# Optimization experiments

Measured on AMD Instinct MI355X. Metric: run time of the kernel, lower is better.

Reference implementation:

```python
import jax, jax.numpy as jnp
import numpy as np

N = 8192          # num_nodes (feature dim == node count, x is square)
H = N // 2        # hidden channels of conv1
NUM_GRAPHS = 8    # graphs in the batch for global_mean_pool
EDGE_P = 0.004    # adjacency density -> avg degree ~33


def setup_inputs() -> dict:
    key = jax.random.key(0)
    kx, kb, k1, k2 = jax.random.split(key, 4)
    # sparse binary adjacency-as-features: nonzero(x) defines the edge list
    x = (jax.random.uniform(kx, (N, N)) < EDGE_P).astype(jnp.float32)
    batch = jnp.sort(jax.random.randint(kb, (N,), 0, NUM_GRAPHS))
    # GCNConv weights (lin has no bias in PyG; separate additive bias)
    W1 = jax.random.normal(k1, (N, H), jnp.float32) / np.sqrt(N)
    b1 = jnp.zeros((H,), jnp.float32)
    W2 = jax.random.normal(k2, (H, N), jnp.float32) / np.sqrt(H)
    b2 = jnp.zeros((N,), jnp.float32)
    return {"x": x, "W1": W1, "b1": b1, "W2": W2, "b2": b2, "batch": batch}


def _gcn_norm_adj(x):
    """Symmetric-normalized adjacency implied by edge_index = nonzero(x).

    PyG GCNConv: edges (r -> c) for every nonzero x[r, c], unit edge weight,
    remaining self loops added, deg = in-degree of target, message to node c is
    deg^-1/2[r] * deg^-1/2[c] * xw[r]. Since x is square/dense we express the
    aggregation as a dense normalized-adjacency matmul (identical math).
    """
    A = (x != 0).astype(x.dtype)                # [N, N], A[r, c] = edge r->c
    idx = jnp.arange(A.shape[0])
    A = A.at[idx, idx].set(1.0)                 # add (remaining) self loops
    deg = A.sum(axis=0)                         # in-degree of each target node
    dinv = jax.lax.rsqrt(deg)                   # deg >= 1 (self loops)
    return dinv[:, None] * A * dinv[None, :]    # B[r, c] = dinv[r]*A[r,c]*dinv[c]


def reference(x, W1, b1, W2, b2, batch):
    B = _gcn_norm_adj(x)
    # conv1: aggregate_c sum_r B[r, c] * (x @ W1)[r]  == B.T @ (x @ W1)
    h = jax.nn.relu(B.T @ (x @ W1) + b1)        # [N, H]
    h = B.T @ (h @ W2) + b2                     # [N, N]
    # global_mean_pool over graph assignment `batch`
    sums = jax.ops.segment_sum(h, batch, num_segments=NUM_GRAPHS)
    cnt = jax.ops.segment_sum(jnp.ones((h.shape[0],), h.dtype), batch,
                              num_segments=NUM_GRAPHS)
    return sums / jnp.maximum(cnt, 1.0)[:, None]  # [NUM_GRAPHS, N]
```

## Files before the change

### kernel.cpp

```cpp
#include <hip/hip_runtime.h>
#include <hip/hip_bf16.h>

#define NN 8192
#define HH 4096
#define GG 8
#define STR 128
#define NCH 32
#define PRG 64
#define FJG 32

typedef unsigned uint4n __attribute__((ext_vector_type(4)));

__device__ inline unsigned bf16rne(float f) {
    unsigned u = __float_as_uint(f);
    unsigned r = 0x7fffu + ((u >> 16) & 1u);
    return (u + r) >> 16;
}
__device__ inline unsigned pack2(float lo, float hi) {
    return bf16rne(lo) | (bf16rne(hi) << 16);
}
__device__ inline void nt_store16(void* p, unsigned a, unsigned b, unsigned c, unsigned d) {
    uint4n v; v.x = a; v.y = b; v.z = c; v.w = d;
    __builtin_nontemporal_store(v, reinterpret_cast<uint4n*>(p));
}
__device__ inline void acc2p(float2& acc, unsigned u) {
    float2 t;
    t.x = __uint_as_float(u << 16);
    t.y = __uint_as_float(u & 0xffff0000u);
    asm("v_pk_add_f32 %0, %1, %0" : "+v"(acc) : "v"(t));
}
__device__ inline void unpack8(uint4 v, float* __restrict__ h) {
    const unsigned* pu = reinterpret_cast<const unsigned*>(&v);
    #pragma unroll
    for (int q = 0; q < 4; ++q) {
        const unsigned u = pu[q];
        h[2 * q]     = __uint_as_float(u << 16);
        h[2 * q + 1] = __uint_as_float(u & 0xffff0000u);
    }
}

__global__ __launch_bounds__(256) void k_cvt(const float* __restrict__ src,
                                             uint4* __restrict__ dst) {
    const size_t i = (size_t)blockIdx.x * 256 + threadIdx.x;
    const float4 a = reinterpret_cast<const float4*>(src)[2 * i];
    const float4 b = reinterpret_cast<const float4*>(src)[2 * i + 1];
    nt_store16(&dst[i], pack2(a.x, a.y), pack2(a.z, a.w),
                        pack2(b.x, b.y), pack2(b.z, b.w));
}

__global__ __launch_bounds__(256) void k_build(const float* __restrict__ x,
                                               unsigned* __restrict__ colfill,
                                               unsigned* __restrict__ degX,
                                               unsigned* __restrict__ degA,
                                               unsigned* __restrict__ csrX,
                                               unsigned* __restrict__ csrA,
                                               unsigned* __restrict__ cscA) {
    const int r = blockIdx.x;
    __shared__ unsigned px, pa;
    if (threadIdx.x == 0) { px = 0u; pa = 0u; }
    __syncthreads();
    const float4* xr = reinterpret_cast<const float4*>(x + (size_t)r * NN);
    #pragma unroll
    for (int i = 0; i < NN / (4 * 256); ++i) {
        const int c4 = i * 256 + threadIdx.x;
        float4 v = xr[c4];
        const float* vp = reinterpret_cast<const float*>(&v);
        #pragma unroll
        for (int k = 0; k < 4; ++k) {
            const int c = c4 * 4 + k;
            const bool nzx = (vp[k] != 0.0f);
            const bool nzA = nzx || (c == r);
            if (nzx) {
                unsigned p = atomicAdd(&px, 1u);
                if (p < STR) csrX[(size_t)r * STR + p] = (unsigned)c << 13;
            }
            if (nzA) {
                unsigned p = atomicAdd(&pa, 1u);
                if (p < STR) csrA[(size_t)r * STR + p] = (unsigned)c;
                unsigned q = atomicAdd(&colfill[c], 1u);
                if (q < STR) cscA[(size_t)c * STR + q] = (unsigned)r << 13;
            }
        }
    }
    __syncthreads();
    if (threadIdx.x == 0) { degX[r] = px; degA[r] = pa; }
}

__global__ __launch_bounds__(256) void k_s(const unsigned* __restrict__ degA,
                                           const unsigned* __restrict__ csrA,
                                           const unsigned* __restrict__ colfill,
                                           const int* __restrict__ batch,
                                           float* __restrict__ s,
                                           unsigned* __restrict__ cnt) {
    const int r = blockIdx.x * 256 + threadIdx.x;
    atomicAdd(&cnt[batch[r]], 1u);
    unsigned deg = degA[r];
    if (deg > STR) deg = STR;
    float bins[GG];
    #pragma unroll
    for (int g = 0; g < GG; ++g) bins[g] = 0.0f;
    for (unsigned e = 0; e < deg; ++e) {
        const unsigned c = csrA[(size_t)r * STR + e];
        const float d = rsqrtf((float)colfill[c]);
        const int gb = batch[c];
        #pragma unroll
        for (int g = 0; g < GG; ++g) bins[g] += (gb == g) ? d : 0.0f;
    }
    const float dr = rsqrtf((float)colfill[r]);
    #pragma unroll
    for (int g = 0; g < GG; ++g) s[(size_t)g * NN + r] = dr * bins[g];
}

__global__ __launch_bounds__(256) void k_spmm1(const char* __restrict__ W1b,
                                               const unsigned* __restrict__ degX,
                                               const unsigned* __restrict__ csrX,
                                               const unsigned* __restrict__ colfill,
                                               unsigned* __restrict__ Mh) {
    const unsigned L = blockIdx.x;
    const int xcd = L & 7;
    const int pix = L >> 3;
    int node = (pix << 2) | (threadIdx.x >> 6);
    node = __builtin_amdgcn_readfirstlane(node);
    const int lane = threadIdx.x & 63;

    unsigned deg = degX[node];
    if (deg > STR) deg = STR;
    const unsigned* __restrict__ el = csrX + (size_t)node * STR;
    const float dr = rsqrtf((float)colfill[node]);

    #pragma unroll
    for (int p = 0; p < 4; ++p) {
        const int ch = xcd + (p << 3);
        const unsigned loff = (unsigned)(ch * 64 + lane) * 4u;
        float2 acc = make_float2(0.f, 0.f);
        unsigned e = 0;
        for (; e + 8 <= deg; e += 8) {
            unsigned o0 = el[e + 0], o1 = el[e + 1], o2 = el[e + 2], o3 = el[e + 3];
            unsigned o4 = el[e + 4], o5 = el[e + 5], o6 = el[e + 6], o7 = el[e + 7];
            const unsigned v0 = *reinterpret_cast<const unsigned*>(W1b + (o0 + loff));
            const unsigned v1 = *reinterpret_cast<const unsigned*>(W1b + (o1 + loff));
            const unsigned v2 = *reinterpret_cast<const unsigned*>(W1b + (o2 + loff));
            const unsigned v3 = *reinterpret_cast<const unsigned*>(W1b + (o3 + loff));
            const unsigned v4 = *reinterpret_cast<const unsigned*>(W1b + (o4 + loff));
            const unsigned v5 = *reinterpret_cast<const unsigned*>(W1b + (o5 + loff));
            const unsigned v6 = *reinterpret_cast<const unsigned*>(W1b + (o6 + loff));
            const unsigned v7 = *reinterpret_cast<const unsigned*>(W1b + (o7 + loff));
            acc2p(acc, v0); acc2p(acc, v1); acc2p(acc, v2); acc2p(acc, v3);
            acc2p(acc, v4); acc2p(acc, v5); acc2p(acc, v6); acc2p(acc, v7);
        }
        for (; e < deg; ++e) {
            unsigned o = el[e];
            acc2p(acc, *reinterpret_cast<const unsigned*>(W1b + (o + loff)));
        }
        __builtin_nontemporal_store(pack2(dr * acc.x, dr * acc.y),
                                    &Mh[(size_t)node * (HH / 2) + ch * 64 + lane]);
    }
}

__global__ __launch_bounds__(256) void k_conv1(const char* __restrict__ Mb,
                                               const float* __restrict__ b1,
                                               const unsigned* __restrict__ colfill,
                                               const unsigned* __restrict__ cscA,
                                               unsigned* __restrict__ hB) {
    const unsigned L = blockIdx.x;
    const int xcd = L & 7;
    const int pix = L >> 3;
    int node = (pix << 2) | (threadIdx.x >> 6);
    node = __builtin_amdgcn_readfirstlane(node);
    const int lane = threadIdx.x & 63;

    unsigned deg = colfill[node];
    const float dc = rsqrtf((float)deg);
    if (deg > STR) deg = STR;
    const unsigned* __restrict__ el = cscA + (size_t)node * STR;

    #pragma unroll
    for (int p = 0; p < 4; ++p) {
        const int ch = xcd + (p << 3);
        const unsigned loff = (unsigned)(ch * 64 + lane) * 4u;
        float2 acc = make_float2(0.f, 0.f);
        unsigned e = 0;
        for (; e + 8 <= deg; e += 8) {
            unsigned o0 = el[e + 0], o1 = el[e + 1], o2 = el[e + 2], o3 = el[e + 3];
            unsigned o4 = el[e + 4], o5 = el[e + 5], o6 = el[e + 6], o7 = el[e + 7];
            const unsigned v0 = *reinterpret_cast<const unsigned*>(Mb + (o0 + loff));
            const unsigned v1 = *reinterpret_cast<const unsigned*>(Mb + (o1 + loff));
            const unsigned v2 = *reinterpret_cast<const unsigned*>(Mb + (o2 + loff));
            const unsigned v3 = *reinterpret_cast<const unsigned*>(Mb + (o3 + loff));
            const unsigned v4 = *reinterpret_cast<const unsigned*>(Mb + (o4 + loff));
            const unsigned v5 = *reinterpret_cast<const unsigned*>(Mb + (o5 + loff));
            const unsigned v6 = *reinterpret_cast<const unsigned*>(Mb + (o6 + loff));
            const unsigned v7 = *reinterpret_cast<const unsigned*>(Mb + (o7 + loff));
            acc2p(acc, v0); acc2p(acc, v1); acc2p(acc, v2); acc2p(acc, v3);
            acc2p(acc, v4); acc2p(acc, v5); acc2p(acc, v6); acc2p(acc, v7);
        }
        for (; e < deg; ++e) {
            unsigned o = el[e];
            acc2p(acc, *reinterpret_cast<const unsigned*>(Mb + (o + loff)));
        }
        const float2 bv = reinterpret_cast<const float2*>(b1)[ch * 64 + lane];
        const float h0 = fmaxf(fmaf(dc, acc.x, bv.x), 0.0f);
        const float h1 = fmaxf(fmaf(dc, acc.y, bv.y), 0.0f);
        __builtin_nontemporal_store(pack2(h0, h1),
                                    &hB[(size_t)node * (HH / 2) + ch * 64 + lane]);
    }
}

__global__ __launch_bounds__(256) void k_poolA(const uint4* __restrict__ hB,
                                               const float* __restrict__ s,
                                               float* __restrict__ part) {
    const int j = blockIdx.x * 256 + threadIdx.x;
    const int c0 = blockIdx.y * (NN / PRG);
    __shared__ float s_t[GG * (NN / PRG)];
    for (int i = threadIdx.x; i < GG * (NN / PRG); i += 256) {
        const int g = i / (NN / PRG);
        const int cc = i % (NN / PRG);
        s_t[i] = s[(size_t)g * NN + c0 + cc];
    }
    __syncthreads();
    float tacc[GG][8];
    #pragma unroll
    for (int g = 0; g < GG; ++g)
        #pragma unroll
        for (int q = 0; q < 8; ++q) tacc[g][q] = 0.0f;
    for (int cc = 0; cc < NN / PRG; ++cc) {
        const uint4 v = hB[(size_t)(c0 + cc) * (HH / 8) + j];
        float hv[8];
        unpack8(v, hv);
        #pragma unroll
        for (int g = 0; g < GG; ++g) {
            const float sv = s_t[g * (NN / PRG) + cc];
            #pragma unroll
            for (int q = 0; q < 8; ++q) tacc[g][q] = fmaf(sv, hv[q], tacc[g][q]);
        }
    }
    float4* p4 = reinterpret_cast<float4*>(part);
    #pragma unroll
    for (int g = 0; g < GG; ++g) {
        const size_t base = ((size_t)(blockIdx.y * GG + g) * HH) / 4 + j * 2;
        p4[base]     = make_float4(tacc[g][0], tacc[g][1], tacc[g][2], tacc[g][3]);
        p4[base + 1] = make_float4(tacc[g][4], tacc[g][5], tacc[g][6], tacc[g][7]);
    }
}

__global__ __launch_bounds__(256) void k_poolB(const float* __restrict__ part,
                                               float* __restrict__ t) {
    const int idx = blockIdx.x * 256 + threadIdx.x;
    const int g = idx / (HH / 4);
    const int j4 = idx % (HH / 4);
    const float4* p4 = reinterpret_cast<const float4*>(part);
    float4 acc = make_float4(0.f, 0.f, 0.f, 0.f);
    for (int rg = 0; rg < PRG; ++rg) {
        const float4 v = p4[((size_t)(rg * GG + g) * HH) / 4 + j4];
        acc.x += v.x; acc.y += v.y; acc.z += v.z; acc.w += v.w;
    }
    reinterpret_cast<float4*>(t)[idx] = acc;
}

__global__ __launch_bounds__(256) void k_final(const float* __restrict__ W2,
                                               const float* __restrict__ t,
                                               const unsigned* __restrict__ cnt,
                                               float* __restrict__ part2) {
    __shared__ float tld[GG * 128];
    const int tj = threadIdx.x;
    const int j0 = blockIdx.y * 128;
    const int nbase = blockIdx.x * 1024;
    for (int i = threadIdx.x; i < GG * 128; i += 256) {
        const int g = i >> 7;
        const int jj = i & 127;
        unsigned c = cnt[g];
        if (c < 1u) c = 1u;
        tld[i] = t[(size_t)g * HH + j0 + jj] * (1.0f / (float)c);
    }
    __syncthreads();
    float4 acc[GG];
    #pragma unroll
    for (int g = 0; g < GG; ++g) acc[g] = make_float4(0.f, 0.f, 0.f, 0.f);
    for (int jj = 0; jj < 128; ++jj) {
        const int jv = j0 + jj;
        float4 w = reinterpret_cast<const float4*>(W2 + (size_t)jv * NN + nbase)[tj];
        #pragma unroll
        for (int g = 0; g < GG; ++g) {
            const float tv = tld[g * 128 + jj];
            acc[g].x = fmaf(tv, w.x, acc[g].x);
            acc[g].y = fmaf(tv, w.y, acc[g].y);
            acc[g].z = fmaf(tv, w.z, acc[g].z);
            acc[g].w = fmaf(tv, w.w, acc[g].w);
        }
    }
    float4* p4 = reinterpret_cast<float4*>(part2);
    #pragma unroll
    for (int g = 0; g < GG; ++g)
        p4[((size_t)(blockIdx.y * GG + g) * NN + nbase) / 4 + tj] = acc[g];
}

__global__ __launch_bounds__(256) void k_fin2(const float* __restrict__ part2,
                                              const float* __restrict__ b2,
                                              float* __restrict__ out) {
    const int idx = blockIdx.x * 256 + threadIdx.x;
    const int g = idx / (NN / 4);
    const int n4 = idx % (NN / 4);
    const float4* p4 = reinterpret_cast<const float4*>(part2);
    float4 acc = reinterpret_cast<const float4*>(b2)[n4];
    for (int jg = 0; jg < FJG; ++jg) {
        const float4 v = p4[((size_t)(jg * GG + g) * NN) / 4 + n4];
        acc.x += v.x; acc.y += v.y; acc.z += v.z; acc.w += v.w;
    }
    reinterpret_cast<float4*>(out)[idx] = acc;
}

extern "C" void kernel_launch(void* const* d_in, const int* in_sizes, int n_in,
                              void* d_out, int out_size, void* d_ws, size_t ws_size,
                              hipStream_t stream) {
    const float* x  = (const float*)d_in[0];
    const float* W1 = (const float*)d_in[1];
    const float* b1 = (const float*)d_in[2];
    const float* W2 = (const float*)d_in[3];
    const float* b2 = (const float*)d_in[4];
    const int* batch = (const int*)d_in[5];
    float* out = (float*)d_out;

    char* ws = (char*)d_ws;
    size_t off = 0;
    auto alloc = [&](size_t bytes) -> char* {
        char* p = ws + off;
        off = (off + bytes + 255) & ~(size_t)255;
        return p;
    };
    uint4*    Mh      = (uint4*)   alloc((size_t)NN * HH * 2);
    uint4*    W1h     = (uint4*)   alloc((size_t)NN * HH * 2);
    uint4*    hB      = W1h;
    char*     zbegin  = ws + off;
    float*    t       = (float*)   alloc((size_t)GG * HH * 4);
    unsigned* colfill = (unsigned*)alloc((size_t)NN * 4);
    unsigned* cnt     = (unsigned*)alloc((size_t)GG * 4);
    char*     zend    = ws + off;
    float*    s       = (float*)   alloc((size_t)GG * NN * 4);
    unsigned* degX    = (unsigned*)alloc((size_t)NN * 4);
    unsigned* degA    = (unsigned*)alloc((size_t)NN * 4);
    unsigned* csrX    = (unsigned*)alloc((size_t)NN * STR * 4);
    unsigned* csrA    = (unsigned*)alloc((size_t)NN * STR * 4);
    unsigned* cscA    = (unsigned*)alloc((size_t)NN * STR * 4);
    float*    part    = (float*)csrX;
    float*    part2   = (float*)csrX;
    (void)ws_size; (void)in_sizes; (void)n_in; (void)out_size;

    hipMemsetAsync(zbegin, 0, (size_t)(zend - zbegin), stream);

    k_cvt<<<(NN * HH / 8) / 256, 256, 0, stream>>>(W1, (uint4*)W1h);
    k_build<<<NN, 256, 0, stream>>>(x, colfill, degX, degA, csrX, csrA, cscA);
    k_s<<<NN / 256, 256, 0, stream>>>(degA, csrA, colfill, batch, s, cnt);
    k_spmm1<<<(NN / 4) * 8, 256, 0, stream>>>((const char*)W1h, degX, csrX, colfill,
                                              (unsigned*)Mh);
    k_conv1<<<(NN / 4) * 8, 256, 0, stream>>>((const char*)Mh, b1, colfill, cscA,
                                              (unsigned*)hB);
    k_poolA<<<dim3(HH / 2048, PRG), 256, 0, stream>>>(hB, s, part);
    k_poolB<<<(GG * HH / 4) / 256, 256, 0, stream>>>(part, t);
    k_final<<<dim3(NN / 1024, FJG), 256, 0, stream>>>(W2, t, cnt, part2);
    k_fin2<<<(GG * NN / 4) / 256, 256, 0, stream>>>(part2, b2, out);
}
```

Before: 693.8 us.

## Merge W1 conversion into build kernel and split SpMM chunks across blocks

Combines the W1 fp32-to-bf16 conversion and the CSR/CSC build into a single launch, with extra blocks past NN doing the conversion. This removes a launch and lets the two independent jobs overlap. The spmm1 and conv1 kernels now give each block one column chunk per node instead of looping over four chunks, so the grid grows 4x. That raises parallelism and memory-level concurrency, but each edge list is now re-read by four separate blocks and the phase-major block order changes cache locality.

```diff
diff --git a/kernel.cpp b/kernel.cpp
--- a/kernel.cpp
+++ b/kernel.cpp
@@ -39,24 +39,26 @@
     }
 }
 
-__global__ __launch_bounds__(256) void k_cvt(const float* __restrict__ src,
-                                             uint4* __restrict__ dst) {
-    const size_t i = (size_t)blockIdx.x * 256 + threadIdx.x;
-    const float4 a = reinterpret_cast<const float4*>(src)[2 * i];
-    const float4 b = reinterpret_cast<const float4*>(src)[2 * i + 1];
-    nt_store16(&dst[i], pack2(a.x, a.y), pack2(a.z, a.w),
-                        pack2(b.x, b.y), pack2(b.z, b.w));
-}
-
-__global__ __launch_bounds__(256) void k_build(const float* __restrict__ x,
+__global__ __launch_bounds__(256) void k_front(const float* __restrict__ x,
+                                               const float* __restrict__ W1,
+                                               uint4* __restrict__ W1h,
                                                unsigned* __restrict__ colfill,
                                                unsigned* __restrict__ degX,
                                                unsigned* __restrict__ degA,
                                                unsigned* __restrict__ csrX,
                                                unsigned* __restrict__ csrA,
                                                unsigned* __restrict__ cscA) {
-    const int r = blockIdx.x;
     __shared__ unsigned px, pa;
+    const int bid = blockIdx.x;
+    if (bid >= NN) {
+        const size_t i = (size_t)(bid - NN) * 256 + threadIdx.x;
+        const float4 a = reinterpret_cast<const float4*>(W1)[2 * i];
+        const float4 b = reinterpret_cast<const float4*>(W1)[2 * i + 1];
+        nt_store16(&W1h[i], pack2(a.x, a.y), pack2(a.z, a.w),
+                            pack2(b.x, b.y), pack2(b.z, b.w));
+        return;
+    }
+    const int r = bid;
     if (threadIdx.x == 0) { px = 0u; pa = 0u; }
     __syncthreads();
     const float4* xr = reinterpret_cast<const float4*>(x + (size_t)r * NN);
@@ -117,8 +119,11 @@
                                                const unsigned* __restrict__ colfill,
                                                unsigned* __restrict__ Mh) {
     const unsigned L = blockIdx.x;
-    const int xcd = L & 7;
-    const int pix = L >> 3;
+    const int xcd   = L & 7;
+    const unsigned k = L >> 3;
+    const int phase = k >> 11;
+    const int pix   = k & 2047;
+    const int ch    = xcd + (phase << 3);
     int node = (pix << 2) | (threadIdx.x >> 6);
     node = __builtin_amdgcn_readfirstlane(node);
     const int lane = threadIdx.x & 63;
@@ -126,35 +131,32 @@
     unsigned deg = degX[node];
     if (deg > STR) deg = STR;
     const unsigned* __restrict__ el = csrX + (size_t)node * STR;
+    const unsigned loff = (unsigned)(ch * 64 + lane) * 4u;
+
+    float2 acc = make_float2(0.f, 0.f);
+    unsigned e = 0;
+    for (; e + 8 <= deg; e += 8) {
+        unsigned o0 = el[e + 0], o1 = el[e + 1], o2 = el[e + 2], o3 = el[e + 3];
+        unsigned o4 = el[e + 4], o5 = el[e + 5], o6 = el[e + 6], o7 = el[e + 7];
+        const unsigned v0 = *reinterpret_cast<const unsigned*>(W1b + (o0 + loff));
+        const unsigned v1 = *reinterpret_cast<const unsigned*>(W1b + (o1 + loff));
+        const unsigned v2 = *reinterpret_cast<const unsigned*>(W1b + (o2 + loff));
+        const unsigned v3 = *reinterpret_cast<const unsigned*>(W1b + (o3 + loff));
+        const unsigned v4 = *reinterpret_cast<const unsigned*>(W1b + (o4 + loff));
+        const unsigned v5 = *reinterpret_cast<const unsigned*>(W1b + (o5 + loff));
+        const unsigned v6 = *reinterpret_cast<const unsigned*>(W1b + (o6 + loff));
+        const unsigned v7 = *reinterpret_cast<const unsigned*>(W1b + (o7 + loff));
+        acc2p(acc, v0); acc2p(acc, v1); acc2p(acc, v2); acc2p(acc, v3);
+        acc2p(acc, v4); acc2p(acc, v5); acc2p(acc, v6); acc2p(acc, v7);
+    }
+    for (; e < deg; ++e) {
+        unsigned o = el[e];
+        acc2p(acc, *reinterpret_cast<const unsigned*>(W1b + (o + loff)));
+    }
+
     const float dr = rsqrtf((float)colfill[node]);
-
-    #pragma unroll
-    for (int p = 0; p < 4; ++p) {
-        const int ch = xcd + (p << 3);
-        const unsigned loff = (unsigned)(ch * 64 + lane) * 4u;
-        float2 acc = make_float2(0.f, 0.f);
-        unsigned e = 0;
-        for (; e + 8 <= deg; e += 8) {
-            unsigned o0 = el[e + 0], o1 = el[e + 1], o2 = el[e + 2], o3 = el[e + 3];
-            unsigned o4 = el[e + 4], o5 = el[e + 5], o6 = el[e + 6], o7 = el[e + 7];
-            const unsigned v0 = *reinterpret_cast<const unsigned*>(W1b + (o0 + loff));
-            const unsigned v1 = *reinterpret_cast<const unsigned*>(W1b + (o1 + loff));
-            const unsigned v2 = *reinterpret_cast<const unsigned*>(W1b + (o2 + loff));
-            const unsigned v3 = *reinterpret_cast<const unsigned*>(W1b + (o3 + loff));
-            const unsigned v4 = *reinterpret_cast<const unsigned*>(W1b + (o4 + loff));
-            const unsigned v5 = *reinterpret_cast<const unsigned*>(W1b + (o5 + loff));
-            const unsigned v6 = *reinterpret_cast<const unsigned*>(W1b + (o6 + loff));
-            const unsigned v7 = *reinterpret_cast<const unsigned*>(W1b + (o7 + loff));
-            acc2p(acc, v0); acc2p(acc, v1); acc2p(acc, v2); acc2p(acc, v3);
-            acc2p(acc, v4); acc2p(acc, v5); acc2p(acc, v6); acc2p(acc, v7);
-        }
-        for (; e < deg; ++e) {
-            unsigned o = el[e];
-            acc2p(acc, *reinterpret_cast<const unsigned*>(W1b + (o + loff)));
-        }
-        __builtin_nontemporal_store(pack2(dr * acc.x, dr * acc.y),
-                                    &Mh[(size_t)node * (HH / 2) + ch * 64 + lane]);
-    }
+    __builtin_nontemporal_store(pack2(dr * acc.x, dr * acc.y),
+                                &Mh[(size_t)node * (HH / 2) + ch * 64 + lane]);
 }
 
 __global__ __launch_bounds__(256) void k_conv1(const char* __restrict__ Mb,
@@ -163,8 +165,11 @@
                                                const unsigned* __restrict__ cscA,
                                                unsigned* __restrict__ hB) {
     const unsigned L = blockIdx.x;
-    const int xcd = L & 7;
-    const int pix = L >> 3;
+    const int xcd   = L & 7;
+    const unsigned k = L >> 3;
+    const int phase = k >> 11;
+    const int pix   = k & 2047;
+    const int ch    = xcd + (phase << 3);
     int node = (pix << 2) | (threadIdx.x >> 6);
     node = __builtin_amdgcn_readfirstlane(node);
     const int lane = threadIdx.x & 63;
@@ -173,37 +178,34 @@
     const float dc = rsqrtf((float)deg);
     if (deg > STR) deg = STR;
     const unsigned* __restrict__ el = cscA + (size_t)node * STR;
-
-    #pragma unroll
-    for (int p = 0; p < 4; ++p) {
-        const int ch = xcd + (p << 3);
-        const unsigned loff = (unsigned)(ch * 64 + lane) * 4u;
-        float2 acc = make_float2(0.f, 0.f);
-        unsigned e = 0;
-        for (; e + 8 <= deg; e += 8) {
-            unsigned o0 = el[e + 0], o1 = el[e + 1], o2 = el[e + 2], o3 = el[e + 3];
-            unsigned o4 = el[e + 4], o5 = el[e + 5], o6 = el[e + 6], o7 = el[e + 7];
-            const unsigned v0 = *reinterpret_cast<const unsigned*>(Mb + (o0 + loff));
-            const unsigned v1 = *reinterpret_cast<const unsigned*>(Mb + (o1 + loff));
-            const unsigned v2 = *reinterpret_cast<const unsigned*>(Mb + (o2 + loff));
-            const unsigned v3 = *reinterpret_cast<const unsigned*>(Mb + (o3 + loff));
-            const unsigned v4 = *reinterpret_cast<const unsigned*>(Mb + (o4 + loff));
-            const unsigned v5 = *reinterpret_cast<const unsigned*>(Mb + (o5 + loff));
-            const unsigned v6 = *reinterpret_cast<const unsigned*>(Mb + (o6 + loff));
-            const unsigned v7 = *reinterpret_cast<const unsigned*>(Mb + (o7 + loff));
-            acc2p(acc, v0); acc2p(acc, v1); acc2p(acc, v2); acc2p(acc, v3);
-            acc2p(acc, v4); acc2p(acc, v5); acc2p(acc, v6); acc2p(acc, v7);
-        }
-        for (; e < deg; ++e) {
-            unsigned o = el[e];
-            acc2p(acc, *reinterpret_cast<const unsigned*>(Mb + (o + loff)));
-        }
-        const float2 bv = reinterpret_cast<const float2*>(b1)[ch * 64 + lane];
-        const float h0 = fmaxf(fmaf(dc, acc.x, bv.x), 0.0f);
-        const float h1 = fmaxf(fmaf(dc, acc.y, bv.y), 0.0f);
-        __builtin_nontemporal_store(pack2(h0, h1),
-                                    &hB[(size_t)node * (HH / 2) + ch * 64 + lane]);
-    }
+    const unsigned loff = (unsigned)(ch * 64 + lane) * 4u;
+
+    float2 acc = make_float2(0.f, 0.f);
+    unsigned e = 0;
+    for (; e + 8 <= deg; e += 8) {
+        unsigned o0 = el[e + 0], o1 = el[e + 1], o2 = el[e + 2], o3 = el[e + 3];
+        unsigned o4 = el[e + 4], o5 = el[e + 5], o6 = el[e + 6], o7 = el[e + 7];
+        const unsigned v0 = *reinterpret_cast<const unsigned*>(Mb + (o0 + loff));
+        const unsigned v1 = *reinterpret_cast<const unsigned*>(Mb + (o1 + loff));
+        const unsigned v2 = *reinterpret_cast<const unsigned*>(Mb + (o2 + loff));
+        const unsigned v3 = *reinterpret_cast<const unsigned*>(Mb + (o3 + loff));
+        const unsigned v4 = *reinterpret_cast<const unsigned*>(Mb + (o4 + loff));
+        const unsigned v5 = *reinterpret_cast<const unsigned*>(Mb + (o5 + loff));
+        const unsigned v6 = *reinterpret_cast<const unsigned*>(Mb + (o6 + loff));
+        const unsigned v7 = *reinterpret_cast<const unsigned*>(Mb + (o7 + loff));
+        acc2p(acc, v0); acc2p(acc, v1); acc2p(acc, v2); acc2p(acc, v3);
+        acc2p(acc, v4); acc2p(acc, v5); acc2p(acc, v6); acc2p(acc, v7);
+    }
+    for (; e < deg; ++e) {
+        unsigned o = el[e];
+        acc2p(acc, *reinterpret_cast<const unsigned*>(Mb + (o + loff)));
+    }
+
+    const float2 bv = reinterpret_cast<const float2*>(b1)[ch * 64 + lane];
+    const float h0 = fmaxf(fmaf(dc, acc.x, bv.x), 0.0f);
+    const float h1 = fmaxf(fmaf(dc, acc.y, bv.y), 0.0f);
+    __builtin_nontemporal_store(pack2(h0, h1),
+                                &hB[(size_t)node * (HH / 2) + ch * 64 + lane]);
 }
 
 __global__ __launch_bounds__(256) void k_poolA(const uint4* __restrict__ hB,
@@ -347,13 +349,13 @@
 
     hipMemsetAsync(zbegin, 0, (size_t)(zend - zbegin), stream);
 
-    k_cvt<<<(NN * HH / 8) / 256, 256, 0, stream>>>(W1, (uint4*)W1h);
-    k_build<<<NN, 256, 0, stream>>>(x, colfill, degX, degA, csrX, csrA, cscA);
+    k_front<<<NN + (NN * HH / 8) / 256, 256, 0, stream>>>(x, W1, (uint4*)W1h, colfill,
+                                                          degX, degA, csrX, csrA, cscA);
     k_s<<<NN / 256, 256, 0, stream>>>(degA, csrA, colfill, batch, s, cnt);
-    k_spmm1<<<(NN / 4) * 8, 256, 0, stream>>>((const char*)W1h, degX, csrX, colfill,
-                                              (unsigned*)Mh);
-    k_conv1<<<(NN / 4) * 8, 256, 0, stream>>>((const char*)Mh, b1, colfill, cscA,
-                                              (unsigned*)hB);
+    k_spmm1<<<(NN / 4) * NCH, 256, 0, stream>>>((const char*)W1h, degX, csrX, colfill,
+                                                (unsigned*)Mh);
+    k_conv1<<<(NN / 4) * NCH, 256, 0, stream>>>((const char*)Mh, b1, colfill, cscA,
+                                                (unsigned*)hB);
     k_poolA<<<dim3(HH / 2048, PRG), 256, 0, stream>>>(hB, s, part);
     k_poolB<<<(GG * HH / 4) / 256, 256, 0, stream>>>(part, t);
     k_final<<<dim3(NN / 1024, FJG), 256, 0, stream>>>(W2, t, cnt, part2);
```

New measurement: 626.5 us. -9.7%, faster.
